# Performance work log

Hardware: AMD Instinct MI355X
Metric: run time of the kernel (lower is better)

## Reference

```python
import jax, jax.numpy as jnp
import numpy as np

BIG = 1e11  # torch code replaces zero counts with 1e11 before dividing
N_LABELS = 5


def _label_mean(state, func):
    """Masked mean per label (1..5). state [..., S, H], func [..., S] int.
    Returns aug [..., 5, H], aug_mask [..., 5] bool. Zero-count labels -> 0
    (sum is exactly 0 and denom is BIG, matching the torch zero-init path)."""
    mask = (func[..., None] == jnp.arange(1, N_LABELS + 1)).astype(state.dtype)  # [...,S,5]
    sums = jnp.einsum('...sl,...sh->...lh', mask, state)                          # [...,5,H]
    counts = mask.sum(axis=-2)                                                    # [...,5]
    aug_mask = counts > 0
    denom = jnp.where(aug_mask, counts, jnp.asarray(BIG, state.dtype))
    return sums / denom[..., None], aug_mask


def _masked_mean(state, func):
    """Mean over all non-pad (func != 0) sentences. state [..., S, H]."""
    m = (func != 0).astype(state.dtype)
    s = jnp.einsum('...s,...sh->...h', m, state)
    c = m.sum(axis=-1)
    pm = c > 0
    denom = jnp.where(pm, c, jnp.asarray(BIG, state.dtype))
    return s / denom[..., None], pm


def setup_inputs() -> dict:
    key = jax.random.key(0)
    k1, k2, k3, k4 = jax.random.split(key, 4)
    B, TS, H = 8, 512, 512       # batch, tar_n_sents, enc_hidden_size
    D, RS = 32, 256              # ref_n_docs, ref_n_sents
    return {
        'tarsent_state': jax.random.normal(k1, (B, TS, H), jnp.float32),
        'tar_func': jax.random.randint(k2, (B, TS), 0, 6),
        'refsent_state': jax.random.normal(k3, (B, D, RS, H), jnp.float32),
        'ref_func': jax.random.randint(k4, (B, D, RS), 0, 6),
    }


def reference(tarsent_state, tar_func, refsent_state, ref_func):
    # tar_aug_state [B,5,H], tar_aug_mask [B,5]
    tar_aug, tar_aug_mask = _label_mean(tarsent_state, tar_func)
    # ref_aug_state [B,D,5,H], ref_aug_mask [B,D,5]
    ref_aug, ref_aug_mask = _label_mean(refsent_state, ref_func)
    # tarpaper_state [B,H], refpaper_state [B,D,H]
    tarpaper_state, tar_mask2 = _masked_mean(tarsent_state, tar_func)
    refpaper_state, ref_mask2 = _masked_mean(refsent_state, ref_func)
    return (tar_aug, tar_aug_mask, ref_aug, ref_aug_mask,
            tarpaper_state, tar_mask2, refpaper_state, ref_mask2)
```

## Files before the change

kernel.cpp:

```cpp
#include <hip/hip_runtime.h>


#define H      512
#define HV     128
#define NL     5
#define BIGF   1e11f
#define CHUNK  64

#define OFF_TAR_AUG       0
#define OFF_TAR_AUG_MASK  20480
#define OFF_REF_AUG       20520
#define OFF_REF_AUG_MASK  675880
#define OFF_TARPAPER      677160
#define OFF_TAR_MASK2     681256
#define OFF_REFPAPER      681264
#define OFF_REF_MASK2     812336

#define NCHUNK_REF 4
#define NCHUNK_TAR 8
#define NBLK_REF   1024
#define NBLK1      1088
#define WSUM_ELEMS ((size_t)NBLK1 * NL * H)
#define WCNT_OFF_B (WSUM_ELEMS * 4)
#define WS_NEED    (WCNT_OFF_B + (size_t)NBLK1 * NL * 4)

__device__ inline float4 f4add(float4 a, float4 b) {
    a.x += b.x; a.y += b.y; a.z += b.z; a.w += b.w; return a;
}
__device__ inline float4 f4scale(float4 a, float s) {
    a.x *= s; a.y *= s; a.z *= s; a.w *= s; return a;
}
__device__ inline float4 f4fma(float w, float4 v, float4 a) {
    a.x = fmaf(w, v.x, a.x); a.y = fmaf(w, v.y, a.y);
    a.z = fmaf(w, v.z, a.z); a.w = fmaf(w, v.w, a.w); return a;
}

__global__ __launch_bounds__(256) void emenc_stage1(
    const float* __restrict__ tar_state, const int* __restrict__ tar_func,
    const float* __restrict__ ref_state, const int* __restrict__ ref_func,
    float* __restrict__ wsum, int* __restrict__ wcnt)
{
    __shared__ float4 spart[HV * NL];
    __shared__ int    crow[CHUNK];
    __shared__ int    clab[CHUNK];
    __shared__ int    scnt5[NL];
    __shared__ int    sm;

    const int b = blockIdx.x;
    const float* state;
    const int*   func;
    int s0;
    if (b < NBLK_REF) {
        const int seg = b >> 2, ch = b & 3;
        state = ref_state + (size_t)seg * 256 * H;
        func  = ref_func  + seg * 256;
        s0    = ch * CHUNK;
    } else {
        const int q = b - NBLK_REF;
        const int seg = q >> 3, ch = q & 7;
        state = tar_state + (size_t)seg * 512 * H;
        func  = tar_func  + seg * 512;
        s0    = ch * CHUNK;
    }

    const int tid = threadIdx.x;

    if (tid < CHUNK) {
        const int l = func[s0 + tid];
        #pragma unroll
        for (int q = 1; q <= NL; ++q) {
            const unsigned long long mq = __ballot(l == q);
            if (tid == 0) scnt5[q - 1] = (int)__popcll(mq);
        }
        const unsigned long long mask = __ballot(l != 0);
        if (l != 0) {
            const int pos = (int)__popcll(mask & ((1ull << tid) - 1ull));
            crow[pos] = s0 + tid;
            clab[pos] = l;
        }
        if (tid == 0) sm = (int)__popcll(mask);
    }
    __syncthreads();

    const int m     = sm;
    const int col   = tid & (HV - 1);
    const int phase = tid >> 7;

    float4 a1 = {0,0,0,0}, a2 = {0,0,0,0}, a3 = {0,0,0,0},
           a4 = {0,0,0,0}, a5 = {0,0,0,0};

    #pragma unroll 4
    for (int r = phase; r < m; r += 2) {
        const int row = crow[r];
        const int l   = clab[r];
        const float4 v = *(const float4*)(state + ((size_t)row << 9) + col * 4);
        a1 = f4fma((l == 1) ? 1.0f : 0.0f, v, a1);
        a2 = f4fma((l == 2) ? 1.0f : 0.0f, v, a2);
        a3 = f4fma((l == 3) ? 1.0f : 0.0f, v, a3);
        a4 = f4fma((l == 4) ? 1.0f : 0.0f, v, a4);
        a5 = f4fma((l == 5) ? 1.0f : 0.0f, v, a5);
    }

    if (phase == 1) {
        spart[col * NL + 0] = a1;
        spart[col * NL + 1] = a2;
        spart[col * NL + 2] = a3;
        spart[col * NL + 3] = a4;
        spart[col * NL + 4] = a5;
    }
    __syncthreads();

    if (phase == 0) {
        a1 = f4add(a1, spart[col * NL + 0]);
        a2 = f4add(a2, spart[col * NL + 1]);
        a3 = f4add(a3, spart[col * NL + 2]);
        a4 = f4add(a4, spart[col * NL + 3]);
        a5 = f4add(a5, spart[col * NL + 4]);

        float* wb = wsum + (size_t)b * NL * H;
        ((float4*)(wb + 0 * H))[col] = a1;
        ((float4*)(wb + 1 * H))[col] = a2;
        ((float4*)(wb + 2 * H))[col] = a3;
        ((float4*)(wb + 3 * H))[col] = a4;
        ((float4*)(wb + 4 * H))[col] = a5;
    }
    if (tid < NL) wcnt[b * NL + tid] = scnt5[tid];
}

__global__ __launch_bounds__(128) void emenc_stage2(
    const float* __restrict__ wsum, const int* __restrict__ wcnt,
    float* __restrict__ out)
{
    const int bb   = blockIdx.x;
    const int seg  = bb / 6;
    const int role = bb - seg * 6;

    int nch, wb0;
    float *aug, *augmask, *paper, *mask2;
    if (seg < 256) {
        nch = NCHUNK_REF; wb0 = seg * NCHUNK_REF;
        aug     = out + OFF_REF_AUG      + (size_t)seg * NL * H;
        augmask = out + OFF_REF_AUG_MASK + seg * NL;
        paper   = out + OFF_REFPAPER     + (size_t)seg * H;
        mask2   = out + OFF_REF_MASK2    + seg;
    } else {
        const int q = seg - 256;
        nch = NCHUNK_TAR; wb0 = NBLK_REF + q * NCHUNK_TAR;
        aug     = out + OFF_TAR_AUG      + (size_t)q * NL * H;
        augmask = out + OFF_TAR_AUG_MASK + q * NL;
        paper   = out + OFF_TARPAPER     + (size_t)q * H;
        mask2   = out + OFF_TAR_MASK2    + q;
    }

    const int col = threadIdx.x;

    if (role < NL) {
        int c = 0;
        for (int ch = 0; ch < nch; ch++) c += wcnt[(wb0 + ch) * NL + role];
        float4 s = {0,0,0,0};
        for (int ch = 0; ch < nch; ch++)
            s = f4add(s, ((const float4*)(wsum + (size_t)(wb0 + ch) * NL * H
                                          + (size_t)role * H))[col]);
        const float inv = 1.0f / (c > 0 ? (float)c : BIGF);
        ((float4*)(aug + (size_t)role * H))[col] = f4scale(s, inv);
        if (col == 0) augmask[role] = c > 0 ? 1.0f : 0.0f;
    } else {
        int ct = 0;
        for (int ch = 0; ch < nch; ch++) {
            #pragma unroll
            for (int l = 0; l < NL; l++) ct += wcnt[(wb0 + ch) * NL + l];
        }
        float4 t = {0,0,0,0};
        for (int ch = 0; ch < nch; ch++) {
            const float4* wb = (const float4*)(wsum + (size_t)(wb0 + ch) * NL * H);
            #pragma unroll
            for (int l = 0; l < NL; l++) t = f4add(t, wb[l * HV + col]);
        }
        ((float4*)paper)[col] = f4scale(t, 1.0f / (ct > 0 ? (float)ct : BIGF));
        if (col == 0) mask2[0] = ct > 0 ? 1.0f : 0.0f;
    }
}

__global__ __launch_bounds__(256) void emenc_single(
    const float* __restrict__ tar_state, const int* __restrict__ tar_func,
    const float* __restrict__ ref_state, const int* __restrict__ ref_func,
    float* __restrict__ out)
{
    __shared__ int    sfunc[512];
    __shared__ float4 spart[HV * NL];
    __shared__ int    scnt[NL];

    const int b = blockIdx.x;
    const float* state;
    const int*   func;
    int S;
    float *aug, *augmask, *paper, *mask2;

    if (b < 256) {
        state   = ref_state + (size_t)b * 256 * H;
        func    = ref_func  + b * 256;
        S       = 256;
        aug     = out + OFF_REF_AUG      + (size_t)b * NL * H;
        augmask = out + OFF_REF_AUG_MASK + b * NL;
        paper   = out + OFF_REFPAPER     + (size_t)b * H;
        mask2   = out + OFF_REF_MASK2    + b;
    } else {
        const int q = b - 256;
        state   = tar_state + (size_t)q * 512 * H;
        func    = tar_func  + q * 512;
        S       = 512;
        aug     = out + OFF_TAR_AUG      + (size_t)q * NL * H;
        augmask = out + OFF_TAR_AUG_MASK + q * NL;
        paper   = out + OFF_TARPAPER     + (size_t)q * H;
        mask2   = out + OFF_TAR_MASK2    + q;
    }

    const int tid = threadIdx.x;
    for (int i = tid; i < S; i += 256) sfunc[i] = func[i];
    __syncthreads();

    const int col   = tid & (HV - 1);
    const int phase = tid >> 7;

    float4 a1 = {0,0,0,0}, a2 = {0,0,0,0}, a3 = {0,0,0,0},
           a4 = {0,0,0,0}, a5 = {0,0,0,0};

    for (int s = phase; s < S; s += 2) {
        float4 v = ((const float4*)(state + (size_t)s * H))[col];
        const int l = sfunc[s];
        a1 = f4fma((l == 1) ? 1.0f : 0.0f, v, a1);
        a2 = f4fma((l == 2) ? 1.0f : 0.0f, v, a2);
        a3 = f4fma((l == 3) ? 1.0f : 0.0f, v, a3);
        a4 = f4fma((l == 4) ? 1.0f : 0.0f, v, a4);
        a5 = f4fma((l == 5) ? 1.0f : 0.0f, v, a5);
    }

    if (phase == 1) {
        spart[col * NL + 0] = a1;
        spart[col * NL + 1] = a2;
        spart[col * NL + 2] = a3;
        spart[col * NL + 3] = a4;
        spart[col * NL + 4] = a5;
    }
    if (tid < NL) {
        int c = 0;
        for (int i = 0; i < S; ++i) c += (sfunc[i] == tid + 1) ? 1 : 0;
        scnt[tid] = c;
    }
    __syncthreads();

    if (phase == 0) {
        a1 = f4add(a1, spart[col * NL + 0]);
        a2 = f4add(a2, spart[col * NL + 1]);
        a3 = f4add(a3, spart[col * NL + 2]);
        a4 = f4add(a4, spart[col * NL + 3]);
        a5 = f4add(a5, spart[col * NL + 4]);

        const int c1 = scnt[0], c2 = scnt[1], c3 = scnt[2],
                  c4 = scnt[3], c5 = scnt[4];
        float4 t  = f4add(f4add(f4add(a1, a2), f4add(a3, a4)), a5);
        const int ct = c1 + c2 + c3 + c4 + c5;

        ((float4*)(aug + 0 * H))[col] = f4scale(a1, 1.0f / (c1 > 0 ? (float)c1 : BIGF));
        ((float4*)(aug + 1 * H))[col] = f4scale(a2, 1.0f / (c2 > 0 ? (float)c2 : BIGF));
        ((float4*)(aug + 2 * H))[col] = f4scale(a3, 1.0f / (c3 > 0 ? (float)c3 : BIGF));
        ((float4*)(aug + 3 * H))[col] = f4scale(a4, 1.0f / (c4 > 0 ? (float)c4 : BIGF));
        ((float4*)(aug + 4 * H))[col] = f4scale(a5, 1.0f / (c5 > 0 ? (float)c5 : BIGF));
        ((float4*)paper)[col]         = f4scale(t,  1.0f / (ct > 0 ? (float)ct : BIGF));

        if (col == 0) {
            augmask[0] = c1 > 0 ? 1.0f : 0.0f;
            augmask[1] = c2 > 0 ? 1.0f : 0.0f;
            augmask[2] = c3 > 0 ? 1.0f : 0.0f;
            augmask[3] = c4 > 0 ? 1.0f : 0.0f;
            augmask[4] = c5 > 0 ? 1.0f : 0.0f;
            mask2[0]   = ct > 0 ? 1.0f : 0.0f;
        }
    }
}

extern "C" void kernel_launch(void* const* d_in, const int* in_sizes, int n_in,
                              void* d_out, int out_size, void* d_ws, size_t ws_size,
                              hipStream_t stream) {
    const float* tar_state = (const float*)d_in[0];
    const int*   tar_func  = (const int*)d_in[1];
    const float* ref_state = (const float*)d_in[2];
    const int*   ref_func  = (const int*)d_in[3];
    float* out = (float*)d_out;

    if (ws_size >= WS_NEED) {
        float* wsum = (float*)d_ws;
        int*   wcnt = (int*)((char*)d_ws + WCNT_OFF_B);
        emenc_stage1<<<NBLK1, 256, 0, stream>>>(tar_state, tar_func,
                                                ref_state, ref_func, wsum, wcnt);
        emenc_stage2<<<264 * 6, 128, 0, stream>>>(wsum, wcnt, out);
    } else {
        emenc_single<<<264, 256, 0, stream>>>(tar_state, tar_func,
                                              ref_state, ref_func, out);
    }
}
```

Before: 207.7 us.

## Fuse two-stage reduction into one kernel split over hidden-dimension slices

Replaces the row-chunked partial-sum kernel plus reduction kernel with one kernel where each block owns a segment and a 128-wide slice of the hidden dimension. Each block compacts all non-pad rows of its segment with wave ballots, then 8 warp-phases accumulate label sums and combine them in shared memory. This removes the workspace round trip and the second launch. In exchange, each block redundantly scans the segment's labels and row compaction is serialized over up to 8 ballot iterations.

```diff
diff --git a/kernel.cpp b/kernel.cpp
--- a/kernel.cpp
+++ b/kernel.cpp
@@ -1,11 +1,9 @@
 #include <hip/hip_runtime.h>
 
 
-#define H      512
-#define HV     128
-#define NL     5
-#define BIGF   1e11f
-#define CHUNK  64
+#define H       512
+#define NL      5
+#define BIGF    1e11f
 
 #define OFF_TAR_AUG       0
 #define OFF_TAR_AUG_MASK  20480
@@ -16,13 +14,13 @@
 #define OFF_REFPAPER      681264
 #define OFF_REF_MASK2     812336
 
-#define NCHUNK_REF 4
-#define NCHUNK_TAR 8
-#define NBLK_REF   1024
-#define NBLK1      1088
-#define WSUM_ELEMS ((size_t)NBLK1 * NL * H)
-#define WCNT_OFF_B (WSUM_ELEMS * 4)
-#define WS_NEED    (WCNT_OFF_B + (size_t)NBLK1 * NL * 4)
+#define NSEG_REF 256
+#define NSEG     264
+#define NSLICE   4
+#define SLICE_F  128
+#define SLICE_V  32
+#define NPHASE   8
+#define SMAX     512
 
 __device__ inline float4 f4add(float4 a, float4 b) {
     a.x += b.x; a.y += b.y; a.z += b.z; a.w += b.w; return a;
@@ -35,177 +33,34 @@
     a.z = fmaf(w, v.z, a.z); a.w = fmaf(w, v.w, a.w); return a;
 }
 
-__global__ __launch_bounds__(256) void emenc_stage1(
+__global__ __launch_bounds__(256) void emenc_fused(
     const float* __restrict__ tar_state, const int* __restrict__ tar_func,
     const float* __restrict__ ref_state, const int* __restrict__ ref_func,
-    float* __restrict__ wsum, int* __restrict__ wcnt)
+    float* __restrict__ out)
 {
-    __shared__ float4 spart[HV * NL];
-    __shared__ int    crow[CHUNK];
-    __shared__ int    clab[CHUNK];
+    __shared__ int    crow[SMAX];
+    __shared__ float4 spart[NPHASE][NL][SLICE_V];
     __shared__ int    scnt5[NL];
     __shared__ int    sm;
 
-    const int b = blockIdx.x;
+    const int b     = blockIdx.x;
+    const int seg   = b >> 2;
+    const int slice = b & 3;
+
     const float* state;
     const int*   func;
-    int s0;
-    if (b < NBLK_REF) {
-        const int seg = b >> 2, ch = b & 3;
-        state = ref_state + (size_t)seg * 256 * H;
-        func  = ref_func  + seg * 256;
-        s0    = ch * CHUNK;
-    } else {
-        const int q = b - NBLK_REF;
-        const int seg = q >> 3, ch = q & 7;
-        state = tar_state + (size_t)seg * 512 * H;
-        func  = tar_func  + seg * 512;
-        s0    = ch * CHUNK;
-    }
-
-    const int tid = threadIdx.x;
-
-    if (tid < CHUNK) {
-        const int l = func[s0 + tid];
-        #pragma unroll
-        for (int q = 1; q <= NL; ++q) {
-            const unsigned long long mq = __ballot(l == q);
-            if (tid == 0) scnt5[q - 1] = (int)__popcll(mq);
-        }
-        const unsigned long long mask = __ballot(l != 0);
-        if (l != 0) {
-            const int pos = (int)__popcll(mask & ((1ull << tid) - 1ull));
-            crow[pos] = s0 + tid;
-            clab[pos] = l;
-        }
-        if (tid == 0) sm = (int)__popcll(mask);
-    }
-    __syncthreads();
-
-    const int m     = sm;
-    const int col   = tid & (HV - 1);
-    const int phase = tid >> 7;
-
-    float4 a1 = {0,0,0,0}, a2 = {0,0,0,0}, a3 = {0,0,0,0},
-           a4 = {0,0,0,0}, a5 = {0,0,0,0};
-
-    #pragma unroll 4
-    for (int r = phase; r < m; r += 2) {
-        const int row = crow[r];
-        const int l   = clab[r];
-        const float4 v = *(const float4*)(state + ((size_t)row << 9) + col * 4);
-        a1 = f4fma((l == 1) ? 1.0f : 0.0f, v, a1);
-        a2 = f4fma((l == 2) ? 1.0f : 0.0f, v, a2);
-        a3 = f4fma((l == 3) ? 1.0f : 0.0f, v, a3);
-        a4 = f4fma((l == 4) ? 1.0f : 0.0f, v, a4);
-        a5 = f4fma((l == 5) ? 1.0f : 0.0f, v, a5);
-    }
-
-    if (phase == 1) {
-        spart[col * NL + 0] = a1;
-        spart[col * NL + 1] = a2;
-        spart[col * NL + 2] = a3;
-        spart[col * NL + 3] = a4;
-        spart[col * NL + 4] = a5;
-    }
-    __syncthreads();
-
-    if (phase == 0) {
-        a1 = f4add(a1, spart[col * NL + 0]);
-        a2 = f4add(a2, spart[col * NL + 1]);
-        a3 = f4add(a3, spart[col * NL + 2]);
-        a4 = f4add(a4, spart[col * NL + 3]);
-        a5 = f4add(a5, spart[col * NL + 4]);
-
-        float* wb = wsum + (size_t)b * NL * H;
-        ((float4*)(wb + 0 * H))[col] = a1;
-        ((float4*)(wb + 1 * H))[col] = a2;
-        ((float4*)(wb + 2 * H))[col] = a3;
-        ((float4*)(wb + 3 * H))[col] = a4;
-        ((float4*)(wb + 4 * H))[col] = a5;
-    }
-    if (tid < NL) wcnt[b * NL + tid] = scnt5[tid];
-}
-
-__global__ __launch_bounds__(128) void emenc_stage2(
-    const float* __restrict__ wsum, const int* __restrict__ wcnt,
-    float* __restrict__ out)
-{
-    const int bb   = blockIdx.x;
-    const int seg  = bb / 6;
-    const int role = bb - seg * 6;
-
-    int nch, wb0;
+    int S;
     float *aug, *augmask, *paper, *mask2;
-    if (seg < 256) {
-        nch = NCHUNK_REF; wb0 = seg * NCHUNK_REF;
+    if (seg < NSEG_REF) {
+        state   = ref_state + (size_t)seg * 256 * H;
+        func    = ref_func  + seg * 256;
+        S       = 256;
         aug     = out + OFF_REF_AUG      + (size_t)seg * NL * H;
         augmask = out + OFF_REF_AUG_MASK + seg * NL;
         paper   = out + OFF_REFPAPER     + (size_t)seg * H;
         mask2   = out + OFF_REF_MASK2    + seg;
     } else {
-        const int q = seg - 256;
-        nch = NCHUNK_TAR; wb0 = NBLK_REF + q * NCHUNK_TAR;
-        aug     = out + OFF_TAR_AUG      + (size_t)q * NL * H;
-        augmask = out + OFF_TAR_AUG_MASK + q * NL;
-        paper   = out + OFF_TARPAPER     + (size_t)q * H;
-        mask2   = out + OFF_TAR_MASK2    + q;
-    }
-
-    const int col = threadIdx.x;
-
-    if (role < NL) {
-        int c = 0;
-        for (int ch = 0; ch < nch; ch++) c += wcnt[(wb0 + ch) * NL + role];
-        float4 s = {0,0,0,0};
-        for (int ch = 0; ch < nch; ch++)
-            s = f4add(s, ((const float4*)(wsum + (size_t)(wb0 + ch) * NL * H
-                                          + (size_t)role * H))[col]);
-        const float inv = 1.0f / (c > 0 ? (float)c : BIGF);
-        ((float4*)(aug + (size_t)role * H))[col] = f4scale(s, inv);
-        if (col == 0) augmask[role] = c > 0 ? 1.0f : 0.0f;
-    } else {
-        int ct = 0;
-        for (int ch = 0; ch < nch; ch++) {
-            #pragma unroll
-            for (int l = 0; l < NL; l++) ct += wcnt[(wb0 + ch) * NL + l];
-        }
-        float4 t = {0,0,0,0};
-        for (int ch = 0; ch < nch; ch++) {
-            const float4* wb = (const float4*)(wsum + (size_t)(wb0 + ch) * NL * H);
-            #pragma unroll
-            for (int l = 0; l < NL; l++) t = f4add(t, wb[l * HV + col]);
-        }
-        ((float4*)paper)[col] = f4scale(t, 1.0f / (ct > 0 ? (float)ct : BIGF));
-        if (col == 0) mask2[0] = ct > 0 ? 1.0f : 0.0f;
-    }
-}
-
-__global__ __launch_bounds__(256) void emenc_single(
-    const float* __restrict__ tar_state, const int* __restrict__ tar_func,
-    const float* __restrict__ ref_state, const int* __restrict__ ref_func,
-    float* __restrict__ out)
-{
-    __shared__ int    sfunc[512];
-    __shared__ float4 spart[HV * NL];
-    __shared__ int    scnt[NL];
-
-    const int b = blockIdx.x;
-    const float* state;
-    const int*   func;
-    int S;
-    float *aug, *augmask, *paper, *mask2;
-
-    if (b < 256) {
-        state   = ref_state + (size_t)b * 256 * H;
-        func    = ref_func  + b * 256;
-        S       = 256;
-        aug     = out + OFF_REF_AUG      + (size_t)b * NL * H;
-        augmask = out + OFF_REF_AUG_MASK + b * NL;
-        paper   = out + OFF_REFPAPER     + (size_t)b * H;
-        mask2   = out + OFF_REF_MASK2    + b;
-    } else {
-        const int q = b - 256;
+        const int q = seg - NSEG_REF;
         state   = tar_state + (size_t)q * 512 * H;
         func    = tar_func  + q * 512;
         S       = 512;
@@ -216,18 +71,50 @@
     }
 
     const int tid = threadIdx.x;
-    for (int i = tid; i < S; i += 256) sfunc[i] = func[i];
+
+    if (tid < 64) {
+        int cbase = 0;
+        int c1 = 0, c2 = 0, c3 = 0, c4 = 0, c5 = 0;
+        for (int s = tid; s < S; s += 64) {
+            const int l = func[s];
+            const unsigned long long m1 = __ballot(l == 1);
+            const unsigned long long m2 = __ballot(l == 2);
+            const unsigned long long m3 = __ballot(l == 3);
+            const unsigned long long m4 = __ballot(l == 4);
+            const unsigned long long m5 = __ballot(l == 5);
+            const unsigned long long mz = __ballot(l != 0);
+            if (l != 0) {
+                const int pos = cbase +
+                    (int)__popcll(mz & ((1ull << tid) - 1ull));
+                crow[pos] = s | (l << 16);
+            }
+            cbase += (int)__popcll(mz);
+            c1 += (int)__popcll(m1); c2 += (int)__popcll(m2);
+            c3 += (int)__popcll(m3); c4 += (int)__popcll(m4);
+            c5 += (int)__popcll(m5);
+        }
+        if (tid == 0) {
+            scnt5[0] = c1; scnt5[1] = c2; scnt5[2] = c3;
+            scnt5[3] = c4; scnt5[4] = c5;
+            sm = cbase;
+        }
+    }
     __syncthreads();
 
-    const int col   = tid & (HV - 1);
-    const int phase = tid >> 7;
+    const int m     = sm;
+    const int col   = tid & (SLICE_V - 1);
+    const int phase = tid >> 5;
+    const float* sp = state + slice * SLICE_F;
 
     float4 a1 = {0,0,0,0}, a2 = {0,0,0,0}, a3 = {0,0,0,0},
            a4 = {0,0,0,0}, a5 = {0,0,0,0};
 
-    for (int s = phase; s < S; s += 2) {
-        float4 v = ((const float4*)(state + (size_t)s * H))[col];
-        const int l = sfunc[s];
+    #pragma unroll 4
+    for (int r = phase; r < m; r += NPHASE) {
+        const int rc  = crow[r];
+        const int row = rc & 0xffff;
+        const int l   = rc >> 16;
+        const float4 v = ((const float4*)(sp + ((size_t)row << 9)))[col];
         a1 = f4fma((l == 1) ? 1.0f : 0.0f, v, a1);
         a2 = f4fma((l == 2) ? 1.0f : 0.0f, v, a2);
         a3 = f4fma((l == 3) ? 1.0f : 0.0f, v, a3);
@@ -235,40 +122,44 @@
         a5 = f4fma((l == 5) ? 1.0f : 0.0f, v, a5);
     }
 
-    if (phase == 1) {
-        spart[col * NL + 0] = a1;
-        spart[col * NL + 1] = a2;
-        spart[col * NL + 2] = a3;
-        spart[col * NL + 3] = a4;
-        spart[col * NL + 4] = a5;
-    }
-    if (tid < NL) {
-        int c = 0;
-        for (int i = 0; i < S; ++i) c += (sfunc[i] == tid + 1) ? 1 : 0;
-        scnt[tid] = c;
-    }
+    spart[phase][0][col] = a1;
+    spart[phase][1][col] = a2;
+    spart[phase][2][col] = a3;
+    spart[phase][3][col] = a4;
+    spart[phase][4][col] = a5;
     __syncthreads();
 
-    if (phase == 0) {
-        a1 = f4add(a1, spart[col * NL + 0]);
-        a2 = f4add(a2, spart[col * NL + 1]);
-        a3 = f4add(a3, spart[col * NL + 2]);
-        a4 = f4add(a4, spart[col * NL + 3]);
-        a5 = f4add(a5, spart[col * NL + 4]);
+    if (tid < SLICE_V) {
+        float4 s1 = {0,0,0,0}, s2 = {0,0,0,0}, s3 = {0,0,0,0},
+               s4 = {0,0,0,0}, s5 = {0,0,0,0};
+        #pragma unroll
+        for (int p = 0; p < NPHASE; ++p) {
+            s1 = f4add(s1, spart[p][0][tid]);
+            s2 = f4add(s2, spart[p][1][tid]);
+            s3 = f4add(s3, spart[p][2][tid]);
+            s4 = f4add(s4, spart[p][3][tid]);
+            s5 = f4add(s5, spart[p][4][tid]);
+        }
+        const int c1 = scnt5[0], c2 = scnt5[1], c3 = scnt5[2],
+                  c4 = scnt5[3], c5 = scnt5[4];
+        const float4 t  = f4add(f4add(f4add(s1, s2), f4add(s3, s4)), s5);
+        const int    ct = c1 + c2 + c3 + c4 + c5;
 
-        const int c1 = scnt[0], c2 = scnt[1], c3 = scnt[2],
-                  c4 = scnt[3], c5 = scnt[4];
-        float4 t  = f4add(f4add(f4add(a1, a2), f4add(a3, a4)), a5);
-        const int ct = c1 + c2 + c3 + c4 + c5;
+        const int cbase = slice * SLICE_F;
+        ((float4*)(aug + 0 * H + cbase))[tid] =
+            f4scale(s1, 1.0f / (c1 > 0 ? (float)c1 : BIGF));
+        ((float4*)(aug + 1 * H + cbase))[tid] =
+            f4scale(s2, 1.0f / (c2 > 0 ? (float)c2 : BIGF));
+        ((float4*)(aug + 2 * H + cbase))[tid] =
+            f4scale(s3, 1.0f / (c3 > 0 ? (float)c3 : BIGF));
+        ((float4*)(aug + 3 * H + cbase))[tid] =
+            f4scale(s4, 1.0f / (c4 > 0 ? (float)c4 : BIGF));
+        ((float4*)(aug + 4 * H + cbase))[tid] =
+            f4scale(s5, 1.0f / (c5 > 0 ? (float)c5 : BIGF));
+        ((float4*)(paper + cbase))[tid] =
+            f4scale(t, 1.0f / (ct > 0 ? (float)ct : BIGF));
 
-        ((float4*)(aug + 0 * H))[col] = f4scale(a1, 1.0f / (c1 > 0 ? (float)c1 : BIGF));
-        ((float4*)(aug + 1 * H))[col] = f4scale(a2, 1.0f / (c2 > 0 ? (float)c2 : BIGF));
-        ((float4*)(aug + 2 * H))[col] = f4scale(a3, 1.0f / (c3 > 0 ? (float)c3 : BIGF));
-        ((float4*)(aug + 3 * H))[col] = f4scale(a4, 1.0f / (c4 > 0 ? (float)c4 : BIGF));
-        ((float4*)(aug + 4 * H))[col] = f4scale(a5, 1.0f / (c5 > 0 ? (float)c5 : BIGF));
-        ((float4*)paper)[col]         = f4scale(t,  1.0f / (ct > 0 ? (float)ct : BIGF));
-
-        if (col == 0) {
+        if (slice == 0 && tid == 0) {
             augmask[0] = c1 > 0 ? 1.0f : 0.0f;
             augmask[1] = c2 > 0 ? 1.0f : 0.0f;
             augmask[2] = c3 > 0 ? 1.0f : 0.0f;
@@ -287,15 +178,8 @@
     const float* ref_state = (const float*)d_in[2];
     const int*   ref_func  = (const int*)d_in[3];
     float* out = (float*)d_out;
+    (void)d_ws; (void)ws_size;
 
-    if (ws_size >= WS_NEED) {
-        float* wsum = (float*)d_ws;
-        int*   wcnt = (int*)((char*)d_ws + WCNT_OFF_B);
-        emenc_stage1<<<NBLK1, 256, 0, stream>>>(tar_state, tar_func,
-                                                ref_state, ref_func, wsum, wcnt);
-        emenc_stage2<<<264 * 6, 128, 0, stream>>>(wsum, wcnt, out);
-    } else {
-        emenc_single<<<264, 256, 0, stream>>>(tar_state, tar_func,
-                                              ref_state, ref_func, out);
-    }
+    emenc_fused<<<NSEG * NSLICE, 256, 0, stream>>>(tar_state, tar_func,
+                                                   ref_state, ref_func, out);
 }
```

Result: no change. 207.2 us (-0.2%).
